# Optimization experiments

Hardware: AMD Instinct MI355X
Metric: run time of the kernel (lower is better)

## Reference

```python
import jax, jax.numpy as jnp
import numpy as np

N = 50000
E = 1600000
F_IN = 1433      # Cora num_node_features
HID = 16
HEADS = 8
N_CLS = 7        # Cora num_classes
NEG_SLOPE = 0.2  # PyG GATConv default


def gat_layer(x, src, dst, W, att_src, att_dst, num_nodes):
    # x: [N, F_in]; W: [F_in, H*C]; att_*: [H, C]
    H, C = att_src.shape
    h = (x @ W).reshape(num_nodes, H, C)                     # [N, H, C]
    a_s = jnp.einsum('nhc,hc->nh', h, att_src)               # [N, H]
    a_d = jnp.einsum('nhc,hc->nh', h, att_dst)               # [N, H]
    e = jax.nn.leaky_relu(a_s[src] + a_d[dst], negative_slope=NEG_SLOPE)  # [E, H]
    # segment softmax over incoming edges of each dst node
    m = jax.ops.segment_max(e, dst, num_segments=num_nodes)  # [N, H]
    ex = jnp.exp(e - m[dst])
    z = jax.ops.segment_sum(ex, dst, num_segments=num_nodes) # [N, H]
    alpha = ex / z[dst]                                      # [E, H]
    msg = alpha[:, :, None] * h[src]                         # [E, H, C]
    return jax.ops.segment_sum(msg, dst, num_segments=num_nodes)  # [N, H, C]


def setup_inputs() -> dict:
    key = jax.random.key(0)
    ks = jax.random.split(key, 10)
    x = jax.random.normal(ks[0], (N, F_IN), dtype=jnp.float32)
    edge_index = jax.random.randint(ks[1], (2, E), 0, N, dtype=jnp.int64)
    s = 0.05
    return {
        'x': x,
        'edge_index': edge_index,
        'W1': jax.random.normal(ks[2], (F_IN, HEADS * HID), dtype=jnp.float32) * s,
        'att_src1': jax.random.normal(ks[3], (HEADS, HID), dtype=jnp.float32) * s,
        'att_dst1': jax.random.normal(ks[4], (HEADS, HID), dtype=jnp.float32) * s,
        'b1': jnp.zeros((HEADS * HID,), dtype=jnp.float32),
        'W2': jax.random.normal(ks[5], (HEADS * HID, N_CLS), dtype=jnp.float32) * s,
        'att_src2': jax.random.normal(ks[6], (1, N_CLS), dtype=jnp.float32) * s,
        'att_dst2': jax.random.normal(ks[7], (1, N_CLS), dtype=jnp.float32) * s,
        'b2': jnp.zeros((N_CLS,), dtype=jnp.float32),
    }


def reference(x, edge_index, W1, att_src1, att_dst1, b1, W2, att_src2, att_dst2, b2):
    num_nodes = x.shape[0]
    # add self loops (PyG GATConv default add_self_loops=True)
    loop = jnp.arange(num_nodes, dtype=edge_index.dtype)
    src = jnp.concatenate([edge_index[0], loop])
    dst = jnp.concatenate([edge_index[1], loop])
    # layer 1: heads=8, concat -> [N, H*C] + bias, then ELU
    h1 = gat_layer(x, src, dst, W1, att_src1, att_dst1, num_nodes)
    h1 = h1.reshape(num_nodes, -1) + b1
    h1 = jax.nn.elu(h1)
    # layer 2: heads=1, concat=False -> mean over heads (=squeeze) + bias
    h2 = gat_layer(h1, src, dst, W2, att_src2, att_dst2, num_nodes)
    return h2.mean(axis=1) + b2
```

## Files before the change

kernel.cpp:

```cpp
#include <hip/hip_runtime.h>
#include <hip/hip_bf16.h>

#define N_NODES 50000
#define N_EDGES 1600000
#define ET (N_EDGES + N_NODES)
#define F_IN 1433
#define KP 1440
#define NK (KP / 32)
#define HC 128
#define NCLS 7
#define NEG 0.2f
#define CSR_STRIDE 160

typedef __attribute__((ext_vector_type(8))) short short8;
typedef __attribute__((ext_vector_type(4))) float f32x4;

__device__ __forceinline__ unsigned short f2bf(float f) {
    unsigned int u = __float_as_uint(f);
    u += 0x7FFFu + ((u >> 16) & 1u);
    return (unsigned short)(u >> 16);
}
__device__ __forceinline__ float bf2f(unsigned short u) {
    return __uint_as_float(((unsigned int)u) << 16);
}

#define GLDS(gp, lp, SZ) __builtin_amdgcn_global_load_lds( \
    (const __attribute__((address_space(1))) unsigned int*)(gp), \
    (__attribute__((address_space(3))) unsigned int*)(lp), SZ, 0, 0)

__global__ void k_build(const int* __restrict__ ei, int* __restrict__ deg, int* __restrict__ csr) {
    int t = blockIdx.x * 256 + threadIdx.x;
    if (t >= ET) return;
    int s, d;
    if (t < N_EDGES) { s = ei[t]; d = ei[N_EDGES + t]; } else { s = d = t - N_EDGES; }
    int pos = atomicAdd(&deg[d], 1);
    csr[d * CSR_STRIDE + pos] = s;
}

__global__ void k_wt(const float* __restrict__ W1, unsigned short* __restrict__ Wt) {
    int t = blockIdx.x * 256 + threadIdx.x;
    if (t >= HC * KP) return;
    int n = t / KP, k = t - n * KP;
    float v = (k < F_IN) ? W1[(size_t)k * HC + n] : 0.f;
    Wt[(size_t)n * KP + k] = f2bf(v);
}

__global__ __launch_bounds__(256, 2) void k_gemm1(const float* __restrict__ X,
                                                  const unsigned short* __restrict__ Wt,
                                                  const float* __restrict__ atS,
                                                  const float* __restrict__ atD,
                                                  unsigned short* __restrict__ Hb,
                                                  float* __restrict__ aS,
                                                  float* __restrict__ aD) {
    __shared__ float lA[3][128][32];
    __shared__ unsigned short lB[2][128][32];
    const int tid = threadIdx.x;
    const int w = tid >> 6, lane = tid & 63;
    const int l15 = lane & 15, quad = lane >> 4;
    const int rowBase = blockIdx.x * 128;

    const int rh  = lane >> 5;
    const int gq  = (lane & 31) >> 2;
    const int kin = lane & 3;
    const int rowLoc0 = w * 32 + rh;
    const int nOff = lane >> 2;
    const int gB   = lane & 3;

    auto issueA = [&](int kt, int buf) {
#pragma unroll
        for (int i = 0; i < 16; ++i) {
            int rowLoc = rowLoc0 + 2 * i;
            int kidx = kt * 32 + ((gq ^ (rowLoc & 7)) << 2) + kin;
            if (kidx > F_IN - 1) kidx = F_IN - 1;
            int rg = rowBase + rowLoc; if (rg > N_NODES - 1) rg = N_NODES - 1;
            GLDS(X + (size_t)rg * F_IN + kidx, &lA[buf][w * 32 + 2 * i][0], 4);
        }
    };
    auto issueB = [&](int kt, int buf) {
#pragma unroll
        for (int j = 0; j < 2; ++j) {
            int n = w * 32 + j * 16 + nOff;
            int gg = gB ^ (n & 3);
            GLDS(Wt + (size_t)n * KP + kt * 32 + gg * 8, &lB[buf][w * 32 + j * 16][0], 16);
        }
    };

    f32x4 acc[2][8];
#pragma unroll
    for (int m = 0; m < 2; ++m)
#pragma unroll
        for (int i = 0; i < 8; ++i) acc[m][i] = (f32x4){0.f, 0.f, 0.f, 0.f};

    issueB(0, 0);
    issueA(0, 0);
    issueA(1, 1);

    int bufA = 0, bufB = 0;
    for (int kt = 0; kt < NK; ++kt) {
        if (kt + 1 < NK) issueB(kt + 1, bufB ^ 1);
        if (kt + 2 < NK) {
            int bi = bufA + 2; if (bi >= 3) bi -= 3;
            issueA(kt + 2, bi);
            asm volatile("s_waitcnt vmcnt(34)" ::: "memory");
        } else if (kt + 2 == NK) {
            asm volatile("s_waitcnt vmcnt(18)" ::: "memory");
        } else {
            asm volatile("s_waitcnt vmcnt(0)" ::: "memory");
        }
        __builtin_amdgcn_sched_barrier(0);
        __builtin_amdgcn_s_barrier();
        __builtin_amdgcn_sched_barrier(0);

        short8 afrag[2];
#pragma unroll
        for (int m = 0; m < 2; ++m) {
            int rowA = w * 32 + m * 16 + l15;
            int key = rowA & 7;
            int p0 = ((2 * quad) ^ key) << 2;
            int p1 = ((2 * quad + 1) ^ key) << 2;
            f32x4 lo = *reinterpret_cast<const f32x4*>(&lA[bufA][rowA][p0]);
            f32x4 hi = *reinterpret_cast<const f32x4*>(&lA[bufA][rowA][p1]);
            short8 a;
#pragma unroll
            for (int e = 0; e < 4; ++e) { a[e] = (short)f2bf(lo[e]); a[4 + e] = (short)f2bf(hi[e]); }
            afrag[m] = a;
        }
        __builtin_amdgcn_s_setprio(1);
#pragma unroll
        for (int nt = 0; nt < 8; ++nt) {
            int nB = nt * 16 + l15;
            int pos = (quad ^ (nB & 3)) << 3;
            short8 b = *reinterpret_cast<const short8*>(&lB[bufB][nB][pos]);
            acc[0][nt] = __builtin_amdgcn_mfma_f32_16x16x32_bf16(afrag[0], b, acc[0][nt], 0, 0, 0);
            acc[1][nt] = __builtin_amdgcn_mfma_f32_16x16x32_bf16(afrag[1], b, acc[1][nt], 0, 0, 0);
        }
        __builtin_amdgcn_s_setprio(0);
        __builtin_amdgcn_sched_barrier(0);
        __builtin_amdgcn_s_barrier();
        bufA = (bufA == 2) ? 0 : bufA + 1;
        bufB ^= 1;
    }

    unsigned short* lds16 = (unsigned short*)&lA[0][0][0];
#pragma unroll
    for (int m = 0; m < 2; ++m) {
        int row = w * 32 + m * 16 + quad * 4;
#pragma unroll
        for (int nt = 0; nt < 8; ++nt)
#pragma unroll
            for (int r = 0; r < 4; ++r)
                lds16[(row + r) * 128 + nt * 16 + l15] = f2bf(acc[m][nt][r]);
    }
    __syncthreads();

    {
        const int row = tid >> 1, half = tid & 1;
        const int grow = rowBase + row;
        if (grow < N_NODES) {
            const unsigned short* src = &lds16[row * 128 + half * 64];
            uint4 u[8];
#pragma unroll
            for (int q = 0; q < 8; ++q) u[q] = *reinterpret_cast<const uint4*>(src + q * 8);
            uint4* dstp = reinterpret_cast<uint4*>(Hb + (size_t)grow * HC + half * 64);
#pragma unroll
            for (int q = 0; q < 8; ++q) dstp[q] = u[q];
#pragma unroll
            for (int hl = 0; hl < 4; ++hl) {
                int h = half * 4 + hl;
                const float* sv = atS + h * 16;
                const float* dv = atD + h * 16;
                unsigned int dw[8] = {u[2*hl].x, u[2*hl].y, u[2*hl].z, u[2*hl].w,
                                      u[2*hl+1].x, u[2*hl+1].y, u[2*hl+1].z, u[2*hl+1].w};
                float s = 0.f, d = 0.f;
#pragma unroll
                for (int j = 0; j < 8; ++j) {
                    float x = bf2f((unsigned short)(dw[j] & 0xFFFF));
                    float y = bf2f((unsigned short)(dw[j] >> 16));
                    s += x * sv[2 * j] + y * sv[2 * j + 1];
                    d += x * dv[2 * j] + y * dv[2 * j + 1];
                }
                aS[grow * 8 + h] = s;
                aD[grow * 8 + h] = d;
            }
        }
    }
}

__global__ __launch_bounds__(256) void k_agg1(const unsigned short* __restrict__ Hb,
        const float* __restrict__ aS, const float* __restrict__ aD,
        const int* __restrict__ deg, const int* __restrict__ csr,
        const float* __restrict__ b1, float* __restrict__ H1) {
    int wave = threadIdx.x >> 6, lane = threadIdx.x & 63;
    int n = blockIdx.x * 4 + wave;
    if (n >= N_NODES) return;
    const int dg = deg[n];
    const int slot = lane >> 3, h = lane & 7;
    const int off = n * CSR_STRIDE;
    const float adv = aD[n * 8 + h];
    float ax[16];
#pragma unroll
    for (int k = 0; k < 16; ++k) ax[k] = 0.f;
    float z = 0.f;
    for (int base = 0; base < dg; base += 8) {
        int idx = base + slot;
        bool valid = idx < dg;
        int s = csr[off + (valid ? idx : 0)];
        float e = aS[s * 8 + h] + adv;
        e = e > 0.f ? e : NEG * e;
        float w = valid ? __expf(e) : 0.f;
        const uint4* hp = reinterpret_cast<const uint4*>(Hb + (size_t)s * HC + h * 16);
        uint4 u0 = hp[0], u1 = hp[1];
        unsigned int dw[8] = {u0.x, u0.y, u0.z, u0.w, u1.x, u1.y, u1.z, u1.w};
        z += w;
#pragma unroll
        for (int j = 0; j < 8; ++j) {
            ax[2 * j]     += w * bf2f((unsigned short)(dw[j] & 0xFFFF));
            ax[2 * j + 1] += w * bf2f((unsigned short)(dw[j] >> 16));
        }
    }
#pragma unroll
    for (int m = 8; m < 64; m <<= 1) {
        z += __shfl_xor(z, m, 64);
#pragma unroll
        for (int k = 0; k < 16; ++k) ax[k] += __shfl_xor(ax[k], m, 64);
    }
    if (slot == 0) {
        float zinv = 1.f / z;
        float o[16];
#pragma unroll
        for (int k = 0; k < 16; ++k) {
            float v = ax[k] * zinv + b1[h * 16 + k];
            o[k] = v > 0.f ? v : expm1f(v);
        }
        float4* dst = reinterpret_cast<float4*>(H1 + (size_t)n * HC + h * 16);
#pragma unroll
        for (int q = 0; q < 4; ++q)
            dst[q] = make_float4(o[4 * q], o[4 * q + 1], o[4 * q + 2], o[4 * q + 3]);
    }
}

__global__ void k_layer2(const float* __restrict__ H1, const float* __restrict__ W2,
                         const float* __restrict__ atS, const float* __restrict__ atD,
                         float* __restrict__ H2, float* __restrict__ aS2,
                         float* __restrict__ aD2) {
    int t = blockIdx.x * 256 + threadIdx.x;
    int n = t >> 3, sub = t & 7;
    if (n >= N_NODES) return;
    float acc[NCLS];
#pragma unroll
    for (int c = 0; c < NCLS; ++c) acc[c] = 0.f;
    const float* hp = H1 + (size_t)n * HC + sub * 16;
#pragma unroll
    for (int k = 0; k < 16; ++k) {
        float x = hp[k];
        const float* w = W2 + (size_t)(sub * 16 + k) * NCLS;
#pragma unroll
        for (int c = 0; c < NCLS; ++c) acc[c] += x * w[c];
    }
#pragma unroll
    for (int m = 1; m < 8; m <<= 1) {
#pragma unroll
        for (int c = 0; c < NCLS; ++c) acc[c] += __shfl_xor(acc[c], m, 64);
    }
    if (sub == 0) {
        float s = 0.f, d = 0.f;
#pragma unroll
        for (int c = 0; c < NCLS; ++c) {
            H2[(size_t)n * NCLS + c] = acc[c];
            s += acc[c] * atS[c];
            d += acc[c] * atD[c];
        }
        aS2[n] = s; aD2[n] = d;
    }
}

__global__ void k_agg2(const float* __restrict__ H2, const float* __restrict__ aS2,
                       const float* __restrict__ aD2, const int* __restrict__ deg,
                       const int* __restrict__ csr,
                       const float* __restrict__ b2, float* __restrict__ out) {
    int t = blockIdx.x * 256 + threadIdx.x;
    int n = t >> 3, sub = t & 7;
    if (n >= N_NODES) return;
    int off = n * CSR_STRIDE, dg = deg[n];
    int subc = sub < NCLS ? sub : NCLS - 1;
    float adv = aD2[n];
    float z = 0.f, acc = 0.f;
    int i = 0;
    for (; i + 4 <= dg; i += 4) {
        int s0 = csr[off + i], s1 = csr[off + i + 1], s2 = csr[off + i + 2], s3 = csr[off + i + 3];
        float e0 = aS2[s0] + adv, e1 = aS2[s1] + adv, e2 = aS2[s2] + adv, e3 = aS2[s3] + adv;
        float v0 = H2[(size_t)s0 * NCLS + subc];
        float v1 = H2[(size_t)s1 * NCLS + subc];
        float v2 = H2[(size_t)s2 * NCLS + subc];
        float v3 = H2[(size_t)s3 * NCLS + subc];
        e0 = e0 > 0.f ? e0 : NEG * e0;
        e1 = e1 > 0.f ? e1 : NEG * e1;
        e2 = e2 > 0.f ? e2 : NEG * e2;
        e3 = e3 > 0.f ? e3 : NEG * e3;
        float w0 = __expf(e0), w1 = __expf(e1), w2 = __expf(e2), w3 = __expf(e3);
        z += (w0 + w1) + (w2 + w3);
        acc += w0 * v0 + w1 * v1 + w2 * v2 + w3 * v3;
    }
    for (; i < dg; ++i) {
        int s0 = csr[off + i];
        float e0 = aS2[s0] + adv;
        float v0 = H2[(size_t)s0 * NCLS + subc];
        e0 = e0 > 0.f ? e0 : NEG * e0;
        float w0 = __expf(e0);
        z += w0; acc += w0 * v0;
    }
    if (sub < NCLS) out[(size_t)n * NCLS + sub] = acc / z + b2[sub];
}

extern "C" void kernel_launch(void* const* d_in, const int* in_sizes, int n_in,
                              void* d_out, int out_size, void* d_ws, size_t ws_size,
                              hipStream_t stream) {
    const float* X   = (const float*)d_in[0];
    const int*   EI  = (const int*)d_in[1];
    const float* W1  = (const float*)d_in[2];
    const float* at_s1 = (const float*)d_in[3];
    const float* at_d1 = (const float*)d_in[4];
    const float* b1  = (const float*)d_in[5];
    const float* W2  = (const float*)d_in[6];
    const float* at_s2 = (const float*)d_in[7];
    const float* at_d2 = (const float*)d_in[8];
    const float* b2  = (const float*)d_in[9];
    float* out = (float*)d_out;

    char* ws = (char*)d_ws;
    size_t o = 0;
    auto alloc = [&](size_t bytes) { size_t r = o; o += (bytes + 255) & ~(size_t)255; return r; };
    unsigned short* Hb = (unsigned short*)(ws + alloc((size_t)N_NODES * HC * 2));
    float* H1   = (float*)(ws + alloc((size_t)N_NODES * HC * 4));
    float* aS1  = (float*)(ws + alloc((size_t)N_NODES * 8 * 4));
    float* aD1  = (float*)(ws + alloc((size_t)N_NODES * 8 * 4));
    float* H2   = (float*)(ws + alloc((size_t)N_NODES * NCLS * 4));
    float* aS2  = (float*)(ws + alloc((size_t)N_NODES * 4));
    float* aD2  = (float*)(ws + alloc((size_t)N_NODES * 4));
    int*   deg  = (int*)(ws + alloc((size_t)N_NODES * 4));
    int*   csr  = (int*)(ws + alloc((size_t)N_NODES * CSR_STRIDE * 4));
    unsigned short* Wt = (unsigned short*)(ws + alloc((size_t)HC * KP * 2));

    hipMemsetAsync(deg, 0, (size_t)N_NODES * 4, stream);

    k_build  <<<(ET + 255) / 256, 256, 0, stream>>>(EI, deg, csr);
    k_wt     <<<(HC * KP + 255) / 256, 256, 0, stream>>>(W1, Wt);
    k_gemm1  <<<(N_NODES + 127) / 128, 256, 0, stream>>>(X, Wt, at_s1, at_d1, Hb, aS1, aD1);
    k_agg1   <<<(N_NODES + 3) / 4, 256, 0, stream>>>(Hb, aS1, aD1, deg, csr, b1, H1);
    k_layer2 <<<(N_NODES * 8 + 255) / 256, 256, 0, stream>>>(H1, W2, at_s2, at_d2, H2, aS2, aD2);
    k_agg2   <<<(N_NODES * 8 + 255) / 256, 256, 0, stream>>>(H2, aS2, aD2, deg, csr, b2, out);
}
```

Before: 696.9 us.

## Fuse layer-2 projection into layer-1 aggregation and parallelize agg2 over edges

```diff
diff --git a/kernel.cpp b/kernel.cpp
--- a/kernel.cpp
+++ b/kernel.cpp
@@ -189,7 +189,10 @@
 __global__ __launch_bounds__(256) void k_agg1(const unsigned short* __restrict__ Hb,
         const float* __restrict__ aS, const float* __restrict__ aD,
         const int* __restrict__ deg, const int* __restrict__ csr,
-        const float* __restrict__ b1, float* __restrict__ H1) {
+        const float* __restrict__ b1, const float* __restrict__ W2,
+        const float* __restrict__ atS2, const float* __restrict__ atD2,
+        float* __restrict__ H2p, float* __restrict__ aS2, float* __restrict__ aD2) {
+    __shared__ float tmp[4][128];
     int wave = threadIdx.x >> 6, lane = threadIdx.x & 63;
     int n = blockIdx.x * 4 + wave;
     if (n >= N_NODES) return;
@@ -224,92 +227,76 @@
 #pragma unroll
         for (int k = 0; k < 16; ++k) ax[k] += __shfl_xor(ax[k], m, 64);
     }
+    const float zinv = 1.f / z;
+    if (slot == 0) {
+#pragma unroll
+        for (int k = 0; k < 16; ++k) tmp[wave][h * 16 + k] = ax[k] * zinv;
+    }
+    __builtin_amdgcn_s_barrier();
+    const int ch = h * 16 + 2 * slot;
+    float o0 = tmp[wave][ch]     + b1[ch];
+    float o1 = tmp[wave][ch + 1] + b1[ch + 1];
+    o0 = o0 > 0.f ? o0 : expm1f(o0);
+    o1 = o1 > 0.f ? o1 : expm1f(o1);
+    float p[NCLS];
+#pragma unroll
+    for (int c = 0; c < NCLS; ++c)
+        p[c] = o0 * W2[(size_t)ch * NCLS + c] + o1 * W2[(size_t)(ch + 1) * NCLS + c];
+#pragma unroll
+    for (int m = 1; m < 64; m <<= 1) {
+#pragma unroll
+        for (int c = 0; c < NCLS; ++c) p[c] += __shfl_xor(p[c], m, 64);
+    }
+    if (lane == 0) {
+        float s2 = 0.f, d2 = 0.f;
+#pragma unroll
+        for (int c = 0; c < NCLS; ++c) {
+            H2p[(size_t)n * 8 + c] = p[c];
+            s2 += p[c] * atS2[c];
+            d2 += p[c] * atD2[c];
+        }
+        aS2[n] = s2; aD2[n] = d2;
+    }
+}
+
+__global__ __launch_bounds__(256) void k_agg2(const float* __restrict__ H2p,
+        const float* __restrict__ aS2, const float* __restrict__ aD2,
+        const int* __restrict__ deg, const int* __restrict__ csr,
+        const float* __restrict__ b2, float* __restrict__ out) {
+    int t = blockIdx.x * 256 + threadIdx.x;
+    int n = t >> 3, slot = t & 7;
+    if (n >= N_NODES) return;
+    const int off = n * CSR_STRIDE, dg = deg[n];
+    const float adv = aD2[n];
+    float z = 0.f;
+    float acc[NCLS];
+#pragma unroll
+    for (int c = 0; c < NCLS; ++c) acc[c] = 0.f;
+    for (int base = 0; base < dg; base += 8) {
+        int idx = base + slot;
+        bool valid = idx < dg;
+        int s = csr[off + (valid ? idx : 0)];
+        float e = aS2[s] + adv;
+        e = e > 0.f ? e : NEG * e;
+        float w = valid ? __expf(e) : 0.f;
+        const float4* hp = reinterpret_cast<const float4*>(H2p + (size_t)s * 8);
+        float4 u0 = hp[0], u1 = hp[1];
+        z += w;
+        acc[0] += w * u0.x; acc[1] += w * u0.y; acc[2] += w * u0.z; acc[3] += w * u0.w;
+        acc[4] += w * u1.x; acc[5] += w * u1.y; acc[6] += w * u1.z;
+    }
+#pragma unroll
+    for (int m = 1; m < 8; m <<= 1) {
+        z += __shfl_xor(z, m, 64);
+#pragma unroll
+        for (int c = 0; c < NCLS; ++c) acc[c] += __shfl_xor(acc[c], m, 64);
+    }
     if (slot == 0) {
         float zinv = 1.f / z;
-        float o[16];
-#pragma unroll
-        for (int k = 0; k < 16; ++k) {
-            float v = ax[k] * zinv + b1[h * 16 + k];
-            o[k] = v > 0.f ? v : expm1f(v);
-        }
-        float4* dst = reinterpret_cast<float4*>(H1 + (size_t)n * HC + h * 16);
-#pragma unroll
-        for (int q = 0; q < 4; ++q)
-            dst[q] = make_float4(o[4 * q], o[4 * q + 1], o[4 * q + 2], o[4 * q + 3]);
-    }
-}
-
-__global__ void k_layer2(const float* __restrict__ H1, const float* __restrict__ W2,
-                         const float* __restrict__ atS, const float* __restrict__ atD,
-                         float* __restrict__ H2, float* __restrict__ aS2,
-                         float* __restrict__ aD2) {
-    int t = blockIdx.x * 256 + threadIdx.x;
-    int n = t >> 3, sub = t & 7;
-    if (n >= N_NODES) return;
-    float acc[NCLS];
-#pragma unroll
-    for (int c = 0; c < NCLS; ++c) acc[c] = 0.f;
-    const float* hp = H1 + (size_t)n * HC + sub * 16;
-#pragma unroll
-    for (int k = 0; k < 16; ++k) {
-        float x = hp[k];
-        const float* w = W2 + (size_t)(sub * 16 + k) * NCLS;
-#pragma unroll
-        for (int c = 0; c < NCLS; ++c) acc[c] += x * w[c];
-    }
-#pragma unroll
-    for (int m = 1; m < 8; m <<= 1) {
-#pragma unroll
-        for (int c = 0; c < NCLS; ++c) acc[c] += __shfl_xor(acc[c], m, 64);
-    }
-    if (sub == 0) {
-        float s = 0.f, d = 0.f;
-#pragma unroll
-        for (int c = 0; c < NCLS; ++c) {
-            H2[(size_t)n * NCLS + c] = acc[c];
-            s += acc[c] * atS[c];
-            d += acc[c] * atD[c];
-        }
-        aS2[n] = s; aD2[n] = d;
-    }
-}
-
-__global__ void k_agg2(const float* __restrict__ H2, const float* __restrict__ aS2,
-                       const float* __restrict__ aD2, const int* __restrict__ deg,
-                       const int* __restrict__ csr,
-                       const float* __restrict__ b2, float* __restrict__ out) {
-    int t = blockIdx.x * 256 + threadIdx.x;
-    int n = t >> 3, sub = t & 7;
-    if (n >= N_NODES) return;
-    int off = n * CSR_STRIDE, dg = deg[n];
-    int subc = sub < NCLS ? sub : NCLS - 1;
-    float adv = aD2[n];
-    float z = 0.f, acc = 0.f;
-    int i = 0;
-    for (; i + 4 <= dg; i += 4) {
-        int s0 = csr[off + i], s1 = csr[off + i + 1], s2 = csr[off + i + 2], s3 = csr[off + i + 3];
-        float e0 = aS2[s0] + adv, e1 = aS2[s1] + adv, e2 = aS2[s2] + adv, e3 = aS2[s3] + adv;
-        float v0 = H2[(size_t)s0 * NCLS + subc];
-        float v1 = H2[(size_t)s1 * NCLS + subc];
-        float v2 = H2[(size_t)s2 * NCLS + subc];
-        float v3 = H2[(size_t)s3 * NCLS + subc];
-        e0 = e0 > 0.f ? e0 : NEG * e0;
-        e1 = e1 > 0.f ? e1 : NEG * e1;
-        e2 = e2 > 0.f ? e2 : NEG * e2;
-        e3 = e3 > 0.f ? e3 : NEG * e3;
-        float w0 = __expf(e0), w1 = __expf(e1), w2 = __expf(e2), w3 = __expf(e3);
-        z += (w0 + w1) + (w2 + w3);
-        acc += w0 * v0 + w1 * v1 + w2 * v2 + w3 * v3;
-    }
-    for (; i < dg; ++i) {
-        int s0 = csr[off + i];
-        float e0 = aS2[s0] + adv;
-        float v0 = H2[(size_t)s0 * NCLS + subc];
-        e0 = e0 > 0.f ? e0 : NEG * e0;
-        float w0 = __expf(e0);
-        z += w0; acc += w0 * v0;
-    }
-    if (sub < NCLS) out[(size_t)n * NCLS + sub] = acc / z + b2[sub];
+#pragma unroll
+        for (int c = 0; c < NCLS; ++c)
+            out[(size_t)n * NCLS + c] = acc[c] * zinv + b2[c];
+    }
 }
 
 extern "C" void kernel_launch(void* const* d_in, const int* in_sizes, int n_in,
@@ -331,10 +318,9 @@
     size_t o = 0;
     auto alloc = [&](size_t bytes) { size_t r = o; o += (bytes + 255) & ~(size_t)255; return r; };
     unsigned short* Hb = (unsigned short*)(ws + alloc((size_t)N_NODES * HC * 2));
-    float* H1   = (float*)(ws + alloc((size_t)N_NODES * HC * 4));
     float* aS1  = (float*)(ws + alloc((size_t)N_NODES * 8 * 4));
     float* aD1  = (float*)(ws + alloc((size_t)N_NODES * 8 * 4));
-    float* H2   = (float*)(ws + alloc((size_t)N_NODES * NCLS * 4));
+    float* H2p  = (float*)(ws + alloc((size_t)N_NODES * 8 * 4));
     float* aS2  = (float*)(ws + alloc((size_t)N_NODES * 4));
     float* aD2  = (float*)(ws + alloc((size_t)N_NODES * 4));
     int*   deg  = (int*)(ws + alloc((size_t)N_NODES * 4));
@@ -346,7 +332,7 @@
     k_build  <<<(ET + 255) / 256, 256, 0, stream>>>(EI, deg, csr);
     k_wt     <<<(HC * KP + 255) / 256, 256, 0, stream>>>(W1, Wt);
     k_gemm1  <<<(N_NODES + 127) / 128, 256, 0, stream>>>(X, Wt, at_s1, at_d1, Hb, aS1, aD1);
-    k_agg1   <<<(N_NODES + 3) / 4, 256, 0, stream>>>(Hb, aS1, aD1, deg, csr, b1, H1);
-    k_layer2 <<<(N_NODES * 8 + 255) / 256, 256, 0, stream>>>(H1, W2, at_s2, at_d2, H2, aS2, aD2);
-    k_agg2   <<<(N_NODES * 8 + 255) / 256, 256, 0, stream>>>(H2, aS2, aD2, deg, csr, b2, out);
-}
+    k_agg1   <<<(N_NODES + 3) / 4, 256, 0, stream>>>(Hb, aS1, aD1, deg, csr, b1, W2,
+                                                     at_s2, at_d2, H2p, aS2, aD2);
+    k_agg2   <<<(N_NODES * 8 + 255) / 256, 256, 0, stream>>>(H2p, aS2, aD2, deg, csr, b2, out);
+}
```

Result: faster. 649.7 us (-6.8%).
